# Kernel tuning notes

Hardware: AMD Instinct MI355X
Metric: run time of the kernel (lower is better)

## Reference

```python
import jax, jax.numpy as jnp
import numpy as np

B, D, R = 256, 4096, 8
MAX_R = 2 * R - 1  # static upper bound on radius (torch uses data-dependent max)


def setup_inputs() -> dict:
    key = jax.random.key(0)
    ks = jax.random.split(key, 6)
    x = jax.random.randint(ks[0], (B, D), 0, 2).astype(jnp.float32)  # binary spins
    W = jax.random.normal(ks[1], (D, D), jnp.float32) / np.float32(np.sqrt(D))
    b = jax.random.normal(ks[2], (D,), jnp.float32)
    radius_raw = jax.random.randint(ks[3], (B, 1), 0, MAX_R)  # +1 in reference -> [1, 2R-1]
    gumbel_u = jax.random.uniform(ks[4], (B, D), jnp.float32)
    u = jax.random.uniform(ks[5], (B,), jnp.float32)
    return {"x": x, "W": W, "b": b, "radius_raw": radius_raw, "gumbel_u": gumbel_u, "u": u}


def _model(x, W, b):
    # quadratic pseudo-Boolean energy model: per-sample scalar score
    return 0.5 * jnp.einsum('bi,ij,bj->b', x, W, x) + x @ b


def reference(x, W, b, radius_raw, gumbel_u, u):
    radius = radius_raw + 1                                   # [B,1] in [1, 2R-1]
    r_mask = (jnp.arange(MAX_R)[None, :] < radius).astype(x.dtype)  # [B, MAX_R]

    score_x = _model(x, W, b)                                 # [B]
    grad = jax.lax.stop_gradient(
        jax.grad(lambda xx: _model(xx, W, b).sum())(x))       # [B,D], detached

    delta_x = -(2.0 * x - 1.0)
    score_change_x = delta_x * grad / 2.0                     # logits of proposal

    # multinomial without replacement == Gumbel top-k on the logits
    eps = 1e-10
    g = -jnp.log(-jnp.log(jnp.clip(gumbel_u, eps, 1.0 - eps)))
    _, indices = jax.lax.top_k(score_change_x + g, MAX_R)     # [B, MAX_R]

    rows = jnp.arange(B)[:, None]
    cur_bits = x[rows, indices]                               # gather
    new_bits = 1.0 - cur_bits
    y = x.at[rows, indices].set(r_mask * new_bits + (1.0 - r_mask) * cur_bits)

    delta_y = -(2.0 * y - 1.0)
    score_y = _model(y, W, b)
    score_change_y = delta_y * grad / 2.0

    log_pypx = score_y - score_x
    log_tilde_pxpy = -jnp.sum(grad * (y - x), axis=-1)
    log_zxzy = (jax.scipy.special.logsumexp(score_change_x, axis=-1)
                - jax.scipy.special.logsumexp(score_change_y, axis=-1))
    log_acc = jnp.minimum(log_pypx + log_tilde_pxpy + log_zxzy, 0.0)

    accepted = (jnp.exp(log_acc) > u).astype(x.dtype)[:, None]  # [B,1]
    return y * accepted + (1.0 - accepted) * x
```

## Files before the change

kernel.cpp:

```cpp
#include <hip/hip_runtime.h>

#define Bsz 256
#define Dd  4096
#define MAXR 15
#define FMAX 3.402823466e+38f
#define BK 64
#define LSTRIDE 72

typedef short bf16x8 __attribute__((ext_vector_type(8)));
typedef float f32x4  __attribute__((ext_vector_type(4)));

__device__ __forceinline__ unsigned short f2bf(float f) {
    unsigned int u = __float_as_uint(f);
    unsigned int r = (u + 0x7fffu + ((u >> 16) & 1u)) >> 16;
    return (unsigned short)r;
}
__device__ __forceinline__ float bf2f(unsigned short h) {
    return __uint_as_float(((unsigned int)h) << 16);
}

__global__ __launch_bounds__(256) void k_ssym(const float* __restrict__ W,
                                              const float* __restrict__ x,
                                              unsigned short* __restrict__ shi,
                                              unsigned short* __restrict__ slo,
                                              unsigned short* __restrict__ xb) {
    __shared__ float t1[64][68];
    __shared__ float t2[64][68];
    int bid = blockIdx.x;
    int bi = 0;
    while (bid >= 64 - bi) { bid -= 64 - bi; ++bi; }
    const int bj = bi + bid;
    const int i0 = bi * 64, j0 = bj * 64;
    const int tid = threadIdx.x;

    #pragma unroll
    for (int sb = 0; sb < 4; ++sb) {
        int s = sb * 256 + tid;
        int r = s >> 4, q = (s & 15) * 4;
        *(float4*)&t1[r][q] = *(const float4*)(W + (size_t)(i0 + r) * Dd + j0 + q);
        *(float4*)&t2[r][q] = *(const float4*)(W + (size_t)(j0 + r) * Dd + i0 + q);
    }
    __syncthreads();

    const int r = tid >> 2, c0 = (tid & 3) * 16;
    {
        unsigned short vh[16], vl[16];
        #pragma unroll
        for (int k = 0; k < 16; ++k) {
            float s = 0.5f * (t1[r][c0 + k] + t2[c0 + k][r]);
            vh[k] = f2bf(s);
            vl[k] = f2bf(s - bf2f(vh[k]));
        }
        size_t o = (size_t)(i0 + r) * Dd + j0 + c0;
        *(uint4*)(shi + o) = *(const uint4*)&vh[0];
        *(uint4*)(shi + o + 8) = *(const uint4*)&vh[8];
        *(uint4*)(slo + o) = *(const uint4*)&vl[0];
        *(uint4*)(slo + o + 8) = *(const uint4*)&vl[8];
    }
    if (bi != bj) {
        unsigned short vh[16], vl[16];
        #pragma unroll
        for (int k = 0; k < 16; ++k) {
            float s = 0.5f * (t2[r][c0 + k] + t1[c0 + k][r]);
            vh[k] = f2bf(s);
            vl[k] = f2bf(s - bf2f(vh[k]));
        }
        size_t o = (size_t)(j0 + r) * Dd + i0 + c0;
        *(uint4*)(shi + o) = *(const uint4*)&vh[0];
        *(uint4*)(shi + o + 8) = *(const uint4*)&vh[8];
        *(uint4*)(slo + o) = *(const uint4*)&vl[0];
        *(uint4*)(slo + o + 8) = *(const uint4*)&vl[8];
    }

    if (blockIdx.x < 256) {
        const float* xp = x + (size_t)blockIdx.x * 4096;
        unsigned short* xo = xb + (size_t)blockIdx.x * 4096;
        #pragma unroll
        for (int c = 0; c < 4; ++c) {
            int e = c * 1024 + tid * 4;
            float4 v = *(const float4*)(xp + e);
            unsigned short o4[4] = { f2bf(v.x), f2bf(v.y), f2bf(v.z), f2bf(v.w) };
            *(uint2*)(xo + e) = *(const uint2*)o4;
        }
    }
}

__global__ __launch_bounds__(128) void k_gemm(const unsigned short* __restrict__ xb,
                                              const unsigned short* __restrict__ shi,
                                              const unsigned short* __restrict__ slo,
                                              float* __restrict__ part,
                                              int kchunk) {
    __shared__ __align__(16) unsigned short As[64 * LSTRIDE];
    __shared__ __align__(16) unsigned short Bh[64 * LSTRIDE];
    __shared__ __align__(16) unsigned short Bl[64 * LSTRIDE];
    const int tid = threadIdx.x;
    const int n0 = blockIdx.x * 64, m0 = blockIdx.y * 64;
    const int kbase = blockIdx.z * kchunk;
    const int w = tid >> 6, lane = tid & 63;
    const int ln = lane & 15, quad = lane >> 4;

    unsigned ga[4], gb[4];
    int lofs[4];
    #pragma unroll
    for (int j = 0; j < 4; ++j) {
        int s = tid + j * 128;
        int r = s >> 3, g = s & 7;
        ga[j]   = (unsigned)((m0 + r) * Dd + kbase + g * 8);
        gb[j]   = (unsigned)((n0 + r) * Dd + kbase + g * 8);
        lofs[j] = r * LSTRIDE + g * 8;
    }

    f32x4 acc[4][2];
    #pragma unroll
    for (int mt = 0; mt < 4; ++mt)
        #pragma unroll
        for (int ct = 0; ct < 2; ++ct)
            #pragma unroll
            for (int rr = 0; rr < 4; ++rr) acc[mt][ct][rr] = 0.0f;

    bf16x8 va[4], vh[4], vl[4];
    #pragma unroll
    for (int j = 0; j < 4; ++j) {
        va[j] = *(const bf16x8*)(xb  + ga[j]);
        vh[j] = *(const bf16x8*)(shi + gb[j]);
        vl[j] = *(const bf16x8*)(slo + gb[j]);
    }

    for (int k0 = 0; k0 < kchunk; k0 += BK) {
        __syncthreads();
        #pragma unroll
        for (int j = 0; j < 4; ++j) {
            *(bf16x8*)&As[lofs[j]] = va[j];
            *(bf16x8*)&Bh[lofs[j]] = vh[j];
            *(bf16x8*)&Bl[lofs[j]] = vl[j];
        }
        {
            int kn = k0 + BK;
            int ks = (kn < kchunk) ? kn : 0;
            #pragma unroll
            for (int j = 0; j < 4; ++j) {
                va[j] = *(const bf16x8*)(xb  + ga[j] + ks);
                vh[j] = *(const bf16x8*)(shi + gb[j] + ks);
                vl[j] = *(const bf16x8*)(slo + gb[j] + ks);
            }
        }
        __syncthreads();
        #pragma unroll
        for (int kk = 0; kk < BK; kk += 32) {
            const int gr = (kk >> 3) + quad;
            bf16x8 a[4];
            #pragma unroll
            for (int mt = 0; mt < 4; ++mt)
                a[mt] = *(const bf16x8*)&As[(mt * 16 + ln) * LSTRIDE + gr * 8];
            #pragma unroll
            for (int ct = 0; ct < 2; ++ct) {
                int rb = w * 32 + ct * 16 + ln;
                bf16x8 bh = *(const bf16x8*)&Bh[rb * LSTRIDE + gr * 8];
                bf16x8 bl = *(const bf16x8*)&Bl[rb * LSTRIDE + gr * 8];
                #pragma unroll
                for (int mt = 0; mt < 4; ++mt) {
                    acc[mt][ct] = __builtin_amdgcn_mfma_f32_16x16x32_bf16(a[mt], bh, acc[mt][ct], 0, 0, 0);
                    acc[mt][ct] = __builtin_amdgcn_mfma_f32_16x16x32_bf16(a[mt], bl, acc[mt][ct], 0, 0, 0);
                }
            }
        }
    }
    float* prow = part + (size_t)blockIdx.z * (Bsz * Dd);
    #pragma unroll
    for (int mt = 0; mt < 4; ++mt)
        #pragma unroll
        for (int ct = 0; ct < 2; ++ct)
            #pragma unroll
            for (int rr = 0; rr < 4; ++rr) {
                int m = m0 + mt * 16 + quad * 4 + rr;
                int n = n0 + w * 32 + ct * 16 + ln;
                prow[(size_t)m * Dd + n] = acc[mt][ct][rr];
            }
}

__device__ __forceinline__ float block_max256(float v, float* redf) {
    #pragma unroll
    for (int off = 32; off; off >>= 1) v = fmaxf(v, __shfl_down(v, off));
    __syncthreads();
    if ((threadIdx.x & 63) == 0) redf[threadIdx.x >> 6] = v;
    __syncthreads();
    return fmaxf(fmaxf(redf[0], redf[1]), fmaxf(redf[2], redf[3]));
}
__device__ __forceinline__ float block_sum256(float v, float* redf) {
    #pragma unroll
    for (int off = 32; off; off >>= 1) v += __shfl_down(v, off);
    __syncthreads();
    if ((threadIdx.x & 63) == 0) redf[threadIdx.x >> 6] = v;
    __syncthreads();
    return (redf[0] + redf[1]) + (redf[2] + redf[3]);
}

__global__ __launch_bounds__(256) void k_epilogue(const float* __restrict__ x,
                                                  const float* __restrict__ W,
                                                  const int* __restrict__ radius_raw,
                                                  const float* __restrict__ gu,
                                                  const float* __restrict__ uvec,
                                                  const float* __restrict__ part,
                                                  const float* __restrict__ bias,
                                                  float* __restrict__ out,
                                                  int nsplit) {
    __shared__ float scx_s[Dd];
    __shared__ float redf[2][4];
    __shared__ int   redi[2][4];
    __shared__ float redsum[4];
    __shared__ int   flips[MAXR];

    const int b = blockIdx.x;
    const int tid = threadIdx.x;
    const float* xrow  = x  + (size_t)b * Dd;
    const float* gurow = gu + (size_t)b * Dd;

    float4 g4[4], bs4[4], xv4[4], uu4[4];
    #pragma unroll
    for (int c = 0; c < 4; ++c) {
        int j = c * 1024 + tid * 4;
        g4[c]  = *(const float4*)(part + (size_t)b * Dd + j);
        bs4[c] = *(const float4*)(bias + j);
        xv4[c] = *(const float4*)(xrow + j);
        uu4[c] = *(const float4*)(gurow + j);
    }
    for (int z = 1; z < nsplit; ++z) {
        const float* pz = part + (size_t)z * (Bsz * Dd) + (size_t)b * Dd;
        #pragma unroll
        for (int c = 0; c < 4; ++c) {
            float4 a = *(const float4*)(pz + c * 1024 + tid * 4);
            g4[c].x += a.x; g4[c].y += a.y; g4[c].z += a.z; g4[c].w += a.w;
        }
    }
    float sc[16], ky[16];
    float lmax = -FMAX;
    float lkey = -FMAX; int lidx = 0x7fffffff;
    #pragma unroll
    for (int c = 0; c < 4; ++c) {
        const float* gg = (const float*)&g4[c];
        const float* gc = (const float*)&bs4[c];
        const float* gx = (const float*)&xv4[c];
        const float* gup = (const float*)&uu4[c];
        #pragma unroll
        for (int e = 0; e < 4; ++e) {
            int r = c * 4 + e;
            float g = gg[e] + gc[e];
            float s = (1.0f - 2.0f * gx[e]) * g * 0.5f;
            float k = s - logf(-logf(fmaxf(gup[e], 1e-10f)));
            sc[r] = s;
            ky[r] = k;
            lmax = fmaxf(lmax, s);
            if (k > lkey) { lkey = k; lidx = c * 1024 + tid * 4 + e; }
        }
        *(float4*)&scx_s[c * 1024 + tid * 4] = *(const float4*)&sc[c * 4];
    }

    float mx = block_max256(lmax, redsum);
    float ls = 0.0f;
    #pragma unroll
    for (int r = 0; r < 16; ++r) ls += expf(sc[r] - mx);
    float sum_x = block_sum256(ls, redsum);
    float lse_x = mx + logf(sum_x);

    const int radius = radius_raw[b] + 1;
    unsigned removed = 0;
    for (int t = 0; t < radius; ++t) {
        float v = lkey; int idx = lidx;
        #pragma unroll
        for (int off = 32; off; off >>= 1) {
            float v2 = __shfl_down(v, off);
            int   i2 = __shfl_down(idx, off);
            if (v2 > v || (v2 == v && i2 < idx)) { v = v2; idx = i2; }
        }
        const int buf = t & 1;
        if ((tid & 63) == 0) { redf[buf][tid >> 6] = v; redi[buf][tid >> 6] = idx; }
        __syncthreads();
        float bv = redf[buf][0]; int bi = redi[buf][0];
        #pragma unroll
        for (int w2 = 1; w2 < 4; ++w2) {
            float v2 = redf[buf][w2]; int i2 = redi[buf][w2];
            if (v2 > bv || (v2 == bv && i2 < bi)) { bv = v2; bi = i2; }
        }
        if (tid == ((bi >> 2) & 255)) {
            removed |= 1u << (((bi >> 10) << 2) | (bi & 3));
            lkey = -FMAX; lidx = 0x7fffffff;
            #pragma unroll
            for (int c = 0; c < 4; ++c)
                #pragma unroll
                for (int e = 0; e < 4; ++e) {
                    int r = c * 4 + e;
                    if (!(removed & (1u << r)) && ky[r] > lkey) {
                        lkey = ky[r]; lidx = c * 1024 + tid * 4 + e;
                    }
                }
        }
        if (tid == 0) flips[t] = bi;
    }
    __syncthreads();

    float delta = 0.0f;
    if (tid < radius) {
        float sv = scx_s[flips[tid]];
        delta = expf(-sv - mx) - expf(sv - mx);
    }
    float sum_y = sum_x + block_sum256(delta, redsum);
    float lse_y = mx + logf(sum_y);

    float ts = 0.0f;
    for (int t = tid; t < radius * radius; t += 256) {
        int p = flips[t / radius], q = flips[t % radius];
        float dp = 1.0f - 2.0f * xrow[p];
        float dq = 1.0f - 2.0f * xrow[q];
        ts += 0.25f * dp * dq * (W[(size_t)p * Dd + q] + W[(size_t)q * Dd + p]);
    }
    float T = block_sum256(ts, redsum);

    float log_acc = fminf(T + lse_x - lse_y, 0.0f);
    int accepted = (expf(log_acc) > uvec[b]) ? 1 : 0;

    float* orow = out + (size_t)b * Dd;
    #pragma unroll
    for (int c = 0; c < 4; ++c)
        *(float4*)(orow + c * 1024 + tid * 4) = xv4[c];
    __syncthreads();
    if (accepted && tid < radius) {
        int p = flips[tid];
        orow[p] = 1.0f - xrow[p];
    }
}

extern "C" void kernel_launch(void* const* d_in, const int* in_sizes, int n_in,
                              void* d_out, int out_size, void* d_ws, size_t ws_size,
                              hipStream_t stream) {
    const float* x          = (const float*)d_in[0];
    const float* W          = (const float*)d_in[1];
    const float* bias       = (const float*)d_in[2];
    const int*   radius_raw = (const int*)d_in[3];
    const float* gu         = (const float*)d_in[4];
    const float* u          = (const float*)d_in[5];
    float* out = (float*)d_out;

    unsigned short* shi = (unsigned short*)d_ws;
    unsigned short* slo = shi + (size_t)Dd * Dd;
    unsigned short* xb  = slo + (size_t)Dd * Dd;
    float*          prt = (float*)(xb + (size_t)Bsz * Dd);

    const size_t fixed = (size_t)2 * Dd * Dd * 2 + (size_t)Bsz * Dd * 2;
    const size_t per_split = (size_t)Bsz * Dd * 4;
    int nsplit = 2;
    if (ws_size >= fixed + 8 * per_split)      nsplit = 8;
    else if (ws_size >= fixed + 4 * per_split) nsplit = 4;
    const int kchunk = Dd / nsplit;

    k_ssym<<<2080, 256, 0, stream>>>(W, x, shi, slo, xb);
    k_gemm<<<dim3(64, 4, nsplit), 128, 0, stream>>>(xb, shi, slo, prt, kchunk);
    k_epilogue<<<Bsz, 256, 0, stream>>>(x, W, radius_raw, gu, u, prt, bias, out, nsplit);
}
```

Measured before the change: 177.6 us.

## Fuse W symmetrization and bf16 split into the GEMM B-tile load

Removes the separate pass that built symmetrized hi/lo bf16 copies of W in workspace. The GEMM now reads fp32 W tiles (row and transposed) directly, symmetrizes and splits them in shared memory, and stages them for the MFMA loop. Each block now covers all 256 batch rows and reads the x operand directly from global memory instead of through LDS. This avoids writing and re-reading 64MB of intermediate data, at the cost of fewer blocks (64×nsplit) and uncoalesced-ish global A-fragment loads.

After: 210.2 us. +18.4%, slower.

```diff
diff --git a/kernel.cpp b/kernel.cpp
--- a/kernel.cpp
+++ b/kernel.cpp
@@ -19,131 +19,77 @@
     return __uint_as_float(((unsigned int)h) << 16);
 }
 
-__global__ __launch_bounds__(256) void k_ssym(const float* __restrict__ W,
-                                              const float* __restrict__ x,
-                                              unsigned short* __restrict__ shi,
-                                              unsigned short* __restrict__ slo,
+__global__ __launch_bounds__(256) void k_xcvt(const float* __restrict__ x,
                                               unsigned short* __restrict__ xb) {
-    __shared__ float t1[64][68];
-    __shared__ float t2[64][68];
-    int bid = blockIdx.x;
-    int bi = 0;
-    while (bid >= 64 - bi) { bid -= 64 - bi; ++bi; }
-    const int bj = bi + bid;
-    const int i0 = bi * 64, j0 = bj * 64;
-    const int tid = threadIdx.x;
-
-    #pragma unroll
-    for (int sb = 0; sb < 4; ++sb) {
-        int s = sb * 256 + tid;
-        int r = s >> 4, q = (s & 15) * 4;
-        *(float4*)&t1[r][q] = *(const float4*)(W + (size_t)(i0 + r) * Dd + j0 + q);
-        *(float4*)&t2[r][q] = *(const float4*)(W + (size_t)(j0 + r) * Dd + i0 + q);
-    }
-    __syncthreads();
-
-    const int r = tid >> 2, c0 = (tid & 3) * 16;
-    {
-        unsigned short vh[16], vl[16];
-        #pragma unroll
-        for (int k = 0; k < 16; ++k) {
-            float s = 0.5f * (t1[r][c0 + k] + t2[c0 + k][r]);
-            vh[k] = f2bf(s);
-            vl[k] = f2bf(s - bf2f(vh[k]));
-        }
-        size_t o = (size_t)(i0 + r) * Dd + j0 + c0;
-        *(uint4*)(shi + o) = *(const uint4*)&vh[0];
-        *(uint4*)(shi + o + 8) = *(const uint4*)&vh[8];
-        *(uint4*)(slo + o) = *(const uint4*)&vl[0];
-        *(uint4*)(slo + o + 8) = *(const uint4*)&vl[8];
-    }
-    if (bi != bj) {
-        unsigned short vh[16], vl[16];
-        #pragma unroll
-        for (int k = 0; k < 16; ++k) {
-            float s = 0.5f * (t2[r][c0 + k] + t1[c0 + k][r]);
-            vh[k] = f2bf(s);
-            vl[k] = f2bf(s - bf2f(vh[k]));
-        }
-        size_t o = (size_t)(j0 + r) * Dd + i0 + c0;
-        *(uint4*)(shi + o) = *(const uint4*)&vh[0];
-        *(uint4*)(shi + o + 8) = *(const uint4*)&vh[8];
-        *(uint4*)(slo + o) = *(const uint4*)&vl[0];
-        *(uint4*)(slo + o + 8) = *(const uint4*)&vl[8];
-    }
-
-    if (blockIdx.x < 256) {
-        const float* xp = x + (size_t)blockIdx.x * 4096;
-        unsigned short* xo = xb + (size_t)blockIdx.x * 4096;
-        #pragma unroll
-        for (int c = 0; c < 4; ++c) {
-            int e = c * 1024 + tid * 4;
-            float4 v = *(const float4*)(xp + e);
-            unsigned short o4[4] = { f2bf(v.x), f2bf(v.y), f2bf(v.z), f2bf(v.w) };
-            *(uint2*)(xo + e) = *(const uint2*)o4;
-        }
-    }
-}
-
-__global__ __launch_bounds__(128) void k_gemm(const unsigned short* __restrict__ xb,
-                                              const unsigned short* __restrict__ shi,
-                                              const unsigned short* __restrict__ slo,
+    int i = (blockIdx.x * 256 + threadIdx.x) * 4;
+    float4 v = *(const float4*)(x + i);
+    unsigned short o4[4] = { f2bf(v.x), f2bf(v.y), f2bf(v.z), f2bf(v.w) };
+    *(uint2*)(xb + i) = *(const uint2*)o4;
+}
+
+__global__ __launch_bounds__(256) void k_gemm(const unsigned short* __restrict__ xb,
+                                              const float* __restrict__ W,
                                               float* __restrict__ part,
                                               int kchunk) {
-    __shared__ __align__(16) unsigned short As[64 * LSTRIDE];
     __shared__ __align__(16) unsigned short Bh[64 * LSTRIDE];
     __shared__ __align__(16) unsigned short Bl[64 * LSTRIDE];
+    __shared__ float Wt[64][68];
     const int tid = threadIdx.x;
-    const int n0 = blockIdx.x * 64, m0 = blockIdx.y * 64;
-    const int kbase = blockIdx.z * kchunk;
+    const int n0 = blockIdx.x * 64;
+    const int kbase = blockIdx.y * kchunk;
     const int w = tid >> 6, lane = tid & 63;
     const int ln = lane & 15, quad = lane >> 4;
-
-    unsigned ga[4], gb[4];
-    int lofs[4];
-    #pragma unroll
-    for (int j = 0; j < 4; ++j) {
-        int s = tid + j * 128;
-        int r = s >> 3, g = s & 7;
-        ga[j]   = (unsigned)((m0 + r) * Dd + kbase + g * 8);
-        gb[j]   = (unsigned)((n0 + r) * Dd + kbase + g * 8);
-        lofs[j] = r * LSTRIDE + g * 8;
-    }
-
-    f32x4 acc[4][2];
+    const int rn = tid >> 2, cb = (tid & 3) * 16;
+
+    f32x4 acc[4][4];
     #pragma unroll
     for (int mt = 0; mt < 4; ++mt)
         #pragma unroll
-        for (int ct = 0; ct < 2; ++ct)
+        for (int ct = 0; ct < 4; ++ct)
             #pragma unroll
             for (int rr = 0; rr < 4; ++rr) acc[mt][ct][rr] = 0.0f;
 
-    bf16x8 va[4], vh[4], vl[4];
-    #pragma unroll
-    for (int j = 0; j < 4; ++j) {
-        va[j] = *(const bf16x8*)(xb  + ga[j]);
-        vh[j] = *(const bf16x8*)(shi + gb[j]);
-        vl[j] = *(const bf16x8*)(slo + gb[j]);
+    float4 w1[4], w2[4];
+    #pragma unroll
+    for (int q = 0; q < 4; ++q) {
+        w1[q] = *(const float4*)(W + (size_t)(n0 + rn) * Dd + kbase + cb + q * 4);
+        w2[q] = *(const float4*)(W + (size_t)(kbase + rn) * Dd + n0 + cb + q * 4);
     }
 
     for (int k0 = 0; k0 < kchunk; k0 += BK) {
+        const int kn = k0 + BK;
+        const int ks = (kn < kchunk) ? kn : 0;
         __syncthreads();
         #pragma unroll
-        for (int j = 0; j < 4; ++j) {
-            *(bf16x8*)&As[lofs[j]] = va[j];
-            *(bf16x8*)&Bh[lofs[j]] = vh[j];
-            *(bf16x8*)&Bl[lofs[j]] = vl[j];
-        }
+        for (int q = 0; q < 4; ++q)
+            *(float4*)&Wt[rn][cb + q * 4] = w2[q];
+        float4 nw2[4];
+        #pragma unroll
+        for (int q = 0; q < 4; ++q)
+            nw2[q] = *(const float4*)(W + (size_t)(kbase + ks + rn) * Dd + n0 + cb + q * 4);
+        __syncthreads();
         {
-            int kn = k0 + BK;
-            int ks = (kn < kchunk) ? kn : 0;
-            #pragma unroll
-            for (int j = 0; j < 4; ++j) {
-                va[j] = *(const bf16x8*)(xb  + ga[j] + ks);
-                vh[j] = *(const bf16x8*)(shi + gb[j] + ks);
-                vl[j] = *(const bf16x8*)(slo + gb[j] + ks);
+            unsigned short vh[16], vl[16];
+            #pragma unroll
+            for (int q = 0; q < 4; ++q) {
+                const float* w1f = (const float*)&w1[q];
+                #pragma unroll
+                for (int e = 0; e < 4; ++e) {
+                    int j = q * 4 + e;
+                    float s = 0.5f * (w1f[e] + Wt[cb + j][rn]);
+                    vh[j] = f2bf(s);
+                    vl[j] = f2bf(s - bf2f(vh[j]));
+                }
             }
-        }
+            *(uint4*)&Bh[rn * LSTRIDE + cb]     = *(const uint4*)&vh[0];
+            *(uint4*)&Bh[rn * LSTRIDE + cb + 8] = *(const uint4*)&vh[8];
+            *(uint4*)&Bl[rn * LSTRIDE + cb]     = *(const uint4*)&vl[0];
+            *(uint4*)&Bl[rn * LSTRIDE + cb + 8] = *(const uint4*)&vl[8];
+        }
+        float4 nw1[4];
+        #pragma unroll
+        for (int q = 0; q < 4; ++q)
+            nw1[q] = *(const float4*)(W + (size_t)(n0 + rn) * Dd + kbase + ks + cb + q * 4);
         __syncthreads();
         #pragma unroll
         for (int kk = 0; kk < BK; kk += 32) {
@@ -151,12 +97,12 @@
             bf16x8 a[4];
             #pragma unroll
             for (int mt = 0; mt < 4; ++mt)
-                a[mt] = *(const bf16x8*)&As[(mt * 16 + ln) * LSTRIDE + gr * 8];
-            #pragma unroll
-            for (int ct = 0; ct < 2; ++ct) {
-                int rb = w * 32 + ct * 16 + ln;
-                bf16x8 bh = *(const bf16x8*)&Bh[rb * LSTRIDE + gr * 8];
-                bf16x8 bl = *(const bf16x8*)&Bl[rb * LSTRIDE + gr * 8];
+                a[mt] = *(const bf16x8*)(xb + (size_t)(w * 64 + mt * 16 + ln) * Dd
+                                            + kbase + k0 + gr * 8);
+            #pragma unroll
+            for (int ct = 0; ct < 4; ++ct) {
+                bf16x8 bh = *(const bf16x8*)&Bh[(ct * 16 + ln) * LSTRIDE + gr * 8];
+                bf16x8 bl = *(const bf16x8*)&Bl[(ct * 16 + ln) * LSTRIDE + gr * 8];
                 #pragma unroll
                 for (int mt = 0; mt < 4; ++mt) {
                     acc[mt][ct] = __builtin_amdgcn_mfma_f32_16x16x32_bf16(a[mt], bh, acc[mt][ct], 0, 0, 0);
@@ -164,16 +110,18 @@
                 }
             }
         }
-    }
-    float* prow = part + (size_t)blockIdx.z * (Bsz * Dd);
+        #pragma unroll
+        for (int q = 0; q < 4; ++q) { w1[q] = nw1[q]; w2[q] = nw2[q]; }
+    }
+    float* prow = part + (size_t)blockIdx.y * (Bsz * Dd);
     #pragma unroll
     for (int mt = 0; mt < 4; ++mt)
         #pragma unroll
-        for (int ct = 0; ct < 2; ++ct)
+        for (int ct = 0; ct < 4; ++ct)
             #pragma unroll
             for (int rr = 0; rr < 4; ++rr) {
-                int m = m0 + mt * 16 + quad * 4 + rr;
-                int n = n0 + w * 32 + ct * 16 + ln;
+                int m = w * 64 + mt * 16 + quad * 4 + rr;
+                int n = n0 + ct * 16 + ln;
                 prow[(size_t)m * Dd + n] = acc[mt][ct][rr];
             }
 }
@@ -340,19 +288,17 @@
     const float* u          = (const float*)d_in[5];
     float* out = (float*)d_out;
 
-    unsigned short* shi = (unsigned short*)d_ws;
-    unsigned short* slo = shi + (size_t)Dd * Dd;
-    unsigned short* xb  = slo + (size_t)Dd * Dd;
+    unsigned short* xb = (unsigned short*)d_ws;
     float*          prt = (float*)(xb + (size_t)Bsz * Dd);
 
-    const size_t fixed = (size_t)2 * Dd * Dd * 2 + (size_t)Bsz * Dd * 2;
+    const size_t fixed = (size_t)Bsz * Dd * 2;
     const size_t per_split = (size_t)Bsz * Dd * 4;
     int nsplit = 2;
     if (ws_size >= fixed + 8 * per_split)      nsplit = 8;
     else if (ws_size >= fixed + 4 * per_split) nsplit = 4;
     const int kchunk = Dd / nsplit;
 
-    k_ssym<<<2080, 256, 0, stream>>>(W, x, shi, slo, xb);
-    k_gemm<<<dim3(64, 4, nsplit), 128, 0, stream>>>(xb, shi, slo, prt, kchunk);
+    k_xcvt<<<(Bsz * Dd) / 1024, 256, 0, stream>>>(x, xb);
+    k_gemm<<<dim3(64, nsplit), 256, 0, stream>>>(xb, W, prt, kchunk);
     k_epilogue<<<Bsz, 256, 0, stream>>>(x, W, radius_raw, gu, u, prt, bias, out, nsplit);
 }
```
